# Kernel tuning notes

Hardware: AMD Instinct MI355X
Metric: run time of the kernel (lower is better)

## Reference

```python
import jax, jax.numpy as jnp
import numpy as np

BS = 4096
D = 256
TAU = 0.5
EPS = 1e-08          # eps added to negative-sum denominator (module arg)
COS_EPS = 1e-08      # nn.CosineSimilarity norm clamp


def setup_inputs() -> dict:
    key = jax.random.key(0)
    k1, k2 = jax.random.split(key)
    zi = jax.random.normal(k1, (BS, D), dtype=jnp.float32)
    zj = jax.random.normal(k2, (BS, D), dtype=jnp.float32)
    return {"zi": zi, "zj": zj}


def reference(zi, zj):
    bs = zi.shape[0]
    n = 2 * bs
    z = jnp.concatenate([zi, zj], axis=0)                       # [2bs, D]
    # cosine similarity = normalized dot products (norms clamped like torch)
    norm = jnp.linalg.norm(z, axis=-1, keepdims=True)
    zn = z / jnp.maximum(norm, COS_EPS)
    sim = jnp.matmul(zn, zn.T) / TAU                            # [2bs, 2bs]
    e = jnp.exp(sim)
    # positive pairs: row i pairs with column (i+bs) mod 2bs
    rows = jnp.arange(n)
    pair = jnp.concatenate([jnp.arange(bs) + bs, jnp.arange(bs)])
    sim_pos = e[rows, pair]                                     # [2bs]
    # negatives: all entries in a row except the diagonal
    sim_neg_sum = e.sum(axis=-1) - jnp.diagonal(e)              # [2bs]
    loss = jnp.mean(-jnp.log(sim_pos / (sim_neg_sum + EPS)))
    return loss
```

## Files before the change

### kernel.cpp

```cpp
#include <hip/hip_runtime.h>
#include <hip/hip_bf16.h>


#define N_ROWS 8192
#define BSZ    4096
#define DIM    256
#define INV_TAU 2.0f
#define EPS_REF 1e-8f
#define COS_EPS 1e-8f
#define NG      128
#define NTT     (NG * (NG + 1) / 2)
#define NBLK    (NTT / 4)

typedef __attribute__((ext_vector_type(4))) float f32x4;
typedef long long i64;
typedef union { int4 v; i64 d[2]; } pack16;

__global__ __launch_bounds__(256) void knorm(const float* __restrict__ zi,
                                             const float* __restrict__ zj,
                                             unsigned char* __restrict__ znsw) {
    __shared__ float lds[4096];
    __shared__ float nrm[16];
    const int rg = blockIdx.x;
    const int t  = threadIdx.x;
    const int row0 = rg * 16;

    #pragma unroll
    for (int s = 0; s < 4; ++s) {
        const int e = s * 1024 + t * 4;
        const int r = row0 + (e >> 8);
        const int k = e & 255;
        const float* src = (r < BSZ) ? zi + (size_t)r * DIM + k
                                     : zj + (size_t)(r - BSZ) * DIM + k;
        *(float4*)&lds[e] = *(const float4*)src;
    }
    __syncthreads();

    {
        const int r = t >> 4, p = t & 15;
        float ss = 0.f;
        #pragma unroll
        for (int j = 0; j < 16; ++j) { const float x = lds[r * 256 + p * 16 + j]; ss += x * x; }
        ss += __shfl_xor(ss, 1); ss += __shfl_xor(ss, 2);
        ss += __shfl_xor(ss, 4); ss += __shfl_xor(ss, 8);
        if (p == 0) nrm[r] = 1.0f / fmaxf(sqrtf(ss), COS_EPS);
    }
    __syncthreads();

    const int kbp = t >> 6, fl = t & 63;
    const int r16 = fl & 15, q = fl >> 4;
    const float inv = nrm[r16];
    int w[4];
    #pragma unroll
    for (int h = 0; h < 2; ++h) {
        const int kk = (2 * kbp + h) * 32 + q * 8;
        float f[8];
        #pragma unroll
        for (int j = 0; j < 8; ++j) f[j] = lds[r16 * 256 + kk + j] * inv;
        int a = 0, b = 0;
        a = __builtin_amdgcn_cvt_pk_fp8_f32(f[0], f[1], a, false);
        a = __builtin_amdgcn_cvt_pk_fp8_f32(f[2], f[3], a, true);
        b = __builtin_amdgcn_cvt_pk_fp8_f32(f[4], f[5], b, false);
        b = __builtin_amdgcn_cvt_pk_fp8_f32(f[6], f[7], b, true);
        w[h * 2] = a; w[h * 2 + 1] = b;
    }
    *(int4*)(znsw + ((size_t)(rg * 4 + kbp) * 64 + fl) * 16) = make_int4(w[0], w[1], w[2], w[3]);
}

__global__ __launch_bounds__(256, 2) void kgemm(const unsigned char* __restrict__ znsw,
                                                float* __restrict__ P,
                                                float* __restrict__ selfdot,
                                                float* __restrict__ pairdot) {
    const int w = threadIdx.x >> 6;
    const int l = threadIdx.x & 63;
    const int t = blockIdx.x * 4 + w;

    int gi = (int)((257.0f - sqrtf(66049.0f - 8.0f * (float)t)) * 0.5f);
    while ((gi + 1) * (257 - (gi + 1)) / 2 <= t) ++gi;
    while (gi * (257 - gi) / 2 > t) --gi;
    const int gj = gi + (t - gi * (257 - gi) / 2);

    const char* abase = (const char*)znsw + (size_t)gi * 16384 + l * 16;
    const char* bbase = (const char*)znsw + (size_t)gj * 16384 + l * 16;

    f32x4 acc[4][4];
    #pragma unroll
    for (int mt = 0; mt < 4; ++mt)
        #pragma unroll
        for (int nt = 0; nt < 4; ++nt)
            acc[mt][nt] = (f32x4){0.f, 0.f, 0.f, 0.f};

    pack16 af[2][4], bfr[2][4];
    #pragma unroll
    for (int mt = 0; mt < 4; ++mt) {
        af[0][mt].v  = *(const int4*)(abase + mt * 4096);
        bfr[0][mt].v = *(const int4*)(bbase + mt * 4096);
    }
    #pragma unroll
    for (int kbp = 0; kbp < 4; ++kbp) {
        const int cur = kbp & 1, nxt = cur ^ 1;
        if (kbp < 3) {
            #pragma unroll
            for (int mt = 0; mt < 4; ++mt) {
                af[nxt][mt].v  = *(const int4*)(abase + mt * 4096 + (kbp + 1) * 1024);
                bfr[nxt][mt].v = *(const int4*)(bbase + mt * 4096 + (kbp + 1) * 1024);
            }
        }
        #pragma unroll
        for (int mt = 0; mt < 4; ++mt)
            #pragma unroll
            for (int nt = 0; nt < 4; ++nt) {
                acc[mt][nt] = __builtin_amdgcn_mfma_f32_16x16x32_fp8_fp8(
                    af[cur][mt].d[0], bfr[cur][nt].d[0], acc[mt][nt], 0, 0, 0);
                acc[mt][nt] = __builtin_amdgcn_mfma_f32_16x16x32_fp8_fp8(
                    af[cur][mt].d[1], bfr[cur][nt].d[1], acc[mt][nt], 0, 0, 0);
            }
    }

    const int c = l & 15, q = l >> 4;
    const int rsel = c - 4 * q;
    const bool vld = (rsel >= 0) && (rsel < 4);

    if (gi == gj || gj == gi + 64) {
        float dv[4];
        #pragma unroll
        for (int mt = 0; mt < 4; ++mt) {
            float d = acc[mt][mt][0];
            #pragma unroll
            for (int r = 1; r < 4; ++r)
                if (rsel == r) d = acc[mt][mt][r];
            dv[mt] = d;
        }
        if (vld) {
            float* dst = (gi == gj) ? selfdot : pairdot;
            #pragma unroll
            for (int mt = 0; mt < 4; ++mt)
                dst[gi * 64 + mt * 16 + c] = dv[mt];
        }
    }

    #pragma unroll
    for (int mt = 0; mt < 4; ++mt)
        #pragma unroll
        for (int nt = 0; nt < 4; ++nt)
            #pragma unroll
            for (int r = 0; r < 4; ++r)
                acc[mt][nt][r] = __expf(acc[mt][nt][r] * INV_TAU);

    float rs[4][4];
    #pragma unroll
    for (int mt = 0; mt < 4; ++mt)
        #pragma unroll
        for (int r = 0; r < 4; ++r)
            rs[mt][r] = acc[mt][0][r] + acc[mt][1][r] + acc[mt][2][r] + acc[mt][3][r];
    #pragma unroll
    for (int off = 1; off <= 8; off <<= 1)
        #pragma unroll
        for (int mt = 0; mt < 4; ++mt)
            #pragma unroll
            for (int r = 0; r < 4; ++r)
                rs[mt][r] += __shfl_xor(rs[mt][r], off);
    if (c == 0) {
        #pragma unroll
        for (int mt = 0; mt < 4; ++mt) {
            const f32x4 o4 = (f32x4){rs[mt][0], rs[mt][1], rs[mt][2], rs[mt][3]};
            __builtin_nontemporal_store(o4,
                (f32x4*)&P[(size_t)gj * N_ROWS + gi * 64 + mt * 16 + q * 4]);
        }
    }

    if (gi != gj) {
        float cs[4];
        #pragma unroll
        for (int nt = 0; nt < 4; ++nt) {
            float s = 0.f;
            #pragma unroll
            for (int mt = 0; mt < 4; ++mt)
                #pragma unroll
                for (int r = 0; r < 4; ++r)
                    s += acc[mt][nt][r];
            s += __shfl_xor(s, 16);
            s += __shfl_xor(s, 32);
            cs[nt] = s;
        }
        if (q == 0) {
            #pragma unroll
            for (int nt = 0; nt < 4; ++nt)
                __builtin_nontemporal_store(cs[nt],
                    &P[(size_t)gi * N_ROWS + gj * 64 + nt * 16 + c]);
        }
    }
}

__global__ __launch_bounds__(256) void kfinal(const float* __restrict__ P,
                                              const float* __restrict__ selfdot,
                                              const float* __restrict__ pairdot,
                                              float* __restrict__ out) {
    const int l = threadIdx.x & 63;
    const int w = threadIdx.x >> 6;
    const int row = blockIdx.x * 64 + l;
    float s = 0.f;
    #pragma unroll
    for (int st = 0; st < 32; ++st)
        s += P[(size_t)(w * 32 + st) * N_ROWS + row];
    __shared__ float wsum[4][64];
    wsum[w][l] = s;
    __syncthreads();
    if (w == 0) {
        const float tot = wsum[0][l] + wsum[1][l] + wsum[2][l] + wsum[3][l];
        const float selfe = __expf(selfdot[row] * INV_TAU);
        const float pd    = pairdot[(row < BSZ) ? row : row - BSZ];
        float loss = logf(tot - selfe + EPS_REF) - pd * INV_TAU;
        #pragma unroll
        for (int off = 32; off >= 1; off >>= 1) loss += __shfl_xor(loss, off);
        if (l == 0) atomicAdd(out, loss * (1.0f / (float)N_ROWS));
    }
}

extern "C" void kernel_launch(void* const* d_in, const int* in_sizes, int n_in,
                              void* d_out, int out_size, void* d_ws, size_t ws_size,
                              hipStream_t stream) {
    const float* zi = (const float*)d_in[0];
    const float* zj = (const float*)d_in[1];
    float* out = (float*)d_out;

    char* ws = (char*)d_ws;
    unsigned char* znsw = (unsigned char*)ws;
    float* P       = (float*)(ws + 2 * 1024 * 1024);
    float* selfdot = (float*)(ws + 6 * 1024 * 1024);
    float* pairdot = (float*)(ws + 6 * 1024 * 1024 + 32 * 1024);

    (void)hipMemsetAsync(out, 0, sizeof(float), stream);
    knorm <<<N_ROWS / 16, 256, 0, stream>>>(zi, zj, znsw);
    kgemm <<<NBLK, 256, 0, stream>>>(znsw, P, selfdot, pairdot);
    kfinal<<<N_ROWS / 64, 256, 0, stream>>>(P, selfdot, pairdot, out);
}
```

Measured before the change: 89.60 us.

## Stage 128-row panels in LDS shared by four waves; fold output zeroing into knorm

The GEMM now gives each block one 128x128 tile of the upper-triangular tile grid. The block stages both fp8 panels into LDS with global_load_lds, and each of its four waves computes one 64x64 quadrant. Each panel is fetched from global memory once per block instead of once per wave, which halves L2/global traffic for the operand loads. In exchange the kernel uses 64KB of LDS per block, which may lower occupancy, and it loses the register double-buffered prefetch, since all loads finish behind a barrier before compute starts. The separate hipMemsetAsync of the output is also replaced by a store in knorm, removing one queue operation.

Result: no change. 89.43 us (-0.2%).

```diff
diff --git a/kernel.cpp b/kernel.cpp
--- a/kernel.cpp
+++ b/kernel.cpp
@@ -8,9 +8,8 @@
 #define INV_TAU 2.0f
 #define EPS_REF 1e-8f
 #define COS_EPS 1e-8f
-#define NG      128
-#define NTT     (NG * (NG + 1) / 2)
-#define NBLK    (NTT / 4)
+#define NG2     64
+#define NBLK2   (NG2 * (NG2 + 1) / 2)
 
 typedef __attribute__((ext_vector_type(4))) float f32x4;
 typedef long long i64;
@@ -18,12 +17,14 @@
 
 __global__ __launch_bounds__(256) void knorm(const float* __restrict__ zi,
                                              const float* __restrict__ zj,
-                                             unsigned char* __restrict__ znsw) {
+                                             unsigned char* __restrict__ znsw,
+                                             float* __restrict__ out) {
     __shared__ float lds[4096];
     __shared__ float nrm[16];
     const int rg = blockIdx.x;
     const int t  = threadIdx.x;
     const int row0 = rg * 16;
+    if (rg == 0 && t == 0) out[0] = 0.f;
 
     #pragma unroll
     for (int s = 0; s < 4; ++s) {
@@ -71,17 +72,33 @@
                                                 float* __restrict__ P,
                                                 float* __restrict__ selfdot,
                                                 float* __restrict__ pairdot) {
+    __shared__ __align__(16) unsigned char pan[2][32768];
     const int w = threadIdx.x >> 6;
     const int l = threadIdx.x & 63;
-    const int t = blockIdx.x * 4 + w;
-
-    int gi = (int)((257.0f - sqrtf(66049.0f - 8.0f * (float)t)) * 0.5f);
-    while ((gi + 1) * (257 - (gi + 1)) / 2 <= t) ++gi;
-    while (gi * (257 - gi) / 2 > t) --gi;
-    const int gj = gi + (t - gi * (257 - gi) / 2);
-
-    const char* abase = (const char*)znsw + (size_t)gi * 16384 + l * 16;
-    const char* bbase = (const char*)znsw + (size_t)gj * 16384 + l * 16;
+
+    const int t = blockIdx.x;
+    int Gi = (int)((129.0f - sqrtf(16641.0f - 8.0f * (float)t)) * 0.5f);
+    while ((Gi + 1) * (129 - (Gi + 1)) / 2 <= t) ++Gi;
+    while (Gi * (129 - Gi) / 2 > t) --Gi;
+    const int Gj = Gi + (t - Gi * (129 - Gi) / 2);
+
+    const char* srcA = (const char*)znsw + (size_t)Gi * 32768;
+    const char* srcB = (const char*)znsw + (size_t)Gj * 32768;
+    #pragma unroll
+    for (int sub = 0; sub < 8; ++sub) {
+        const int off = sub * 4096 + w * 1024;
+        __builtin_amdgcn_global_load_lds(
+            (const __attribute__((address_space(1))) void*)(srcA + off + l * 16),
+            (__attribute__((address_space(3))) void*)(&pan[0][off]), 16, 0, 0);
+        __builtin_amdgcn_global_load_lds(
+            (const __attribute__((address_space(1))) void*)(srcB + off + l * 16),
+            (__attribute__((address_space(3))) void*)(&pan[1][off]), 16, 0, 0);
+    }
+    __syncthreads();
+
+    const int rh = w >> 1, ch = w & 1;
+    const char* Ap = (const char*)&pan[0][0] + rh * 16384 + l * 16;
+    const char* Bp = (const char*)&pan[1][0] + ch * 16384 + l * 16;
 
     f32x4 acc[4][4];
     #pragma unroll
@@ -90,30 +107,21 @@
         for (int nt = 0; nt < 4; ++nt)
             acc[mt][nt] = (f32x4){0.f, 0.f, 0.f, 0.f};
 
-    pack16 af[2][4], bfr[2][4];
-    #pragma unroll
-    for (int mt = 0; mt < 4; ++mt) {
-        af[0][mt].v  = *(const int4*)(abase + mt * 4096);
-        bfr[0][mt].v = *(const int4*)(bbase + mt * 4096);
-    }
     #pragma unroll
     for (int kbp = 0; kbp < 4; ++kbp) {
-        const int cur = kbp & 1, nxt = cur ^ 1;
-        if (kbp < 3) {
-            #pragma unroll
-            for (int mt = 0; mt < 4; ++mt) {
-                af[nxt][mt].v  = *(const int4*)(abase + mt * 4096 + (kbp + 1) * 1024);
-                bfr[nxt][mt].v = *(const int4*)(bbase + mt * 4096 + (kbp + 1) * 1024);
-            }
-        }
+        pack16 a4[4], b4[4];
+        #pragma unroll
+        for (int mt = 0; mt < 4; ++mt) a4[mt].v = *(const int4*)(Ap + (mt * 4 + kbp) * 1024);
+        #pragma unroll
+        for (int nt = 0; nt < 4; ++nt) b4[nt].v = *(const int4*)(Bp + (nt * 4 + kbp) * 1024);
         #pragma unroll
         for (int mt = 0; mt < 4; ++mt)
             #pragma unroll
             for (int nt = 0; nt < 4; ++nt) {
                 acc[mt][nt] = __builtin_amdgcn_mfma_f32_16x16x32_fp8_fp8(
-                    af[cur][mt].d[0], bfr[cur][nt].d[0], acc[mt][nt], 0, 0, 0);
+                    a4[mt].d[0], b4[nt].d[0], acc[mt][nt], 0, 0, 0);
                 acc[mt][nt] = __builtin_amdgcn_mfma_f32_16x16x32_fp8_fp8(
-                    af[cur][mt].d[1], bfr[cur][nt].d[1], acc[mt][nt], 0, 0, 0);
+                    a4[mt].d[1], b4[nt].d[1], acc[mt][nt], 0, 0, 0);
             }
     }
 
@@ -121,7 +129,7 @@
     const int rsel = c - 4 * q;
     const bool vld = (rsel >= 0) && (rsel < 4);
 
-    if (gi == gj || gj == gi + 64) {
+    if ((Gi == Gj || Gj == Gi + 32) && rh == ch) {
         float dv[4];
         #pragma unroll
         for (int mt = 0; mt < 4; ++mt) {
@@ -132,10 +140,10 @@
             dv[mt] = d;
         }
         if (vld) {
-            float* dst = (gi == gj) ? selfdot : pairdot;
+            float* dst = (Gi == Gj) ? selfdot : pairdot;
             #pragma unroll
             for (int mt = 0; mt < 4; ++mt)
-                dst[gi * 64 + mt * 16 + c] = dv[mt];
+                dst[Gi * 128 + rh * 64 + mt * 16 + c] = dv[mt];
         }
     }
 
@@ -165,11 +173,11 @@
         for (int mt = 0; mt < 4; ++mt) {
             const f32x4 o4 = (f32x4){rs[mt][0], rs[mt][1], rs[mt][2], rs[mt][3]};
             __builtin_nontemporal_store(o4,
-                (f32x4*)&P[(size_t)gj * N_ROWS + gi * 64 + mt * 16 + q * 4]);
-        }
-    }
-
-    if (gi != gj) {
+                (f32x4*)&P[(size_t)(Gj * 2 + ch) * N_ROWS + Gi * 128 + rh * 64 + mt * 16 + q * 4]);
+        }
+    }
+
+    if (Gi != Gj) {
         float cs[4];
         #pragma unroll
         for (int nt = 0; nt < 4; ++nt) {
@@ -187,7 +195,7 @@
             #pragma unroll
             for (int nt = 0; nt < 4; ++nt)
                 __builtin_nontemporal_store(cs[nt],
-                    &P[(size_t)gi * N_ROWS + gj * 64 + nt * 16 + c]);
+                    &P[(size_t)(Gi * 2 + rh) * N_ROWS + Gj * 128 + ch * 64 + nt * 16 + c]);
         }
     }
 }
@@ -230,8 +238,7 @@
     float* selfdot = (float*)(ws + 6 * 1024 * 1024);
     float* pairdot = (float*)(ws + 6 * 1024 * 1024 + 32 * 1024);
 
-    (void)hipMemsetAsync(out, 0, sizeof(float), stream);
-    knorm <<<N_ROWS / 16, 256, 0, stream>>>(zi, zj, znsw);
-    kgemm <<<NBLK, 256, 0, stream>>>(znsw, P, selfdot, pairdot);
+    knorm <<<N_ROWS / 16, 256, 0, stream>>>(zi, zj, znsw, out);
+    kgemm <<<NBLK2, 256, 0, stream>>>(znsw, P, selfdot, pairdot);
     kfinal<<<N_ROWS / 64, 256, 0, stream>>>(P, selfdot, pairdot, out);
 }
```
